# Kernel tuning notes

Hardware: AMD Instinct MI355X
Metric: run time of the kernel (lower is better)

The kernel has to match this reference:

```python
import jax, jax.numpy as jnp
import numpy as np

NC, NP, H, E, EL = 4096, 8192, 128, 500000, 500000


def setup_inputs() -> dict:
    key = jax.random.key(0)
    ks = jax.random.split(key, 32)
    W = lambda i, shape: jax.random.normal(ks[i], shape, dtype=jnp.float32) * 0.02
    inp = {
        "x_country": jax.random.normal(ks[0], (NC, NC), dtype=jnp.float32),
        "x_product": jax.random.normal(ks[1], (NP, NP), dtype=jnp.float32),
        # input projections (Linear(num_x, hidden)) and node-id embeddings
        "Wc_lin": W(2, (NC, H)), "bc_lin": jnp.zeros((H,), jnp.float32),
        "Wp_lin": W(3, (NP, H)), "bp_lin": jnp.zeros((H,), jnp.float32),
        "emb_c": W(4, (NC, H)),
        "emb_p": W(5, (NP, H)),
        # SAGEConv params per layer per edge type (lin_l has bias, lin_r does not)
        "W1ep_l": W(6, (H, H)), "b1ep": jnp.zeros((H,), jnp.float32), "W1ep_r": W(7, (H, H)),
        "W1pc_l": W(8, (H, H)), "b1pc": jnp.zeros((H,), jnp.float32), "W1pc_r": W(9, (H, H)),
        "W2ep_l": W(10, (H, H)), "b2ep": jnp.zeros((H,), jnp.float32), "W2ep_r": W(11, (H, H)),
        "W2pc_l": W(12, (H, H)), "b2pc": jnp.zeros((H,), jnp.float32), "W2pc_r": W(13, (H, H)),
        # graph structure
        "nid_c": jnp.arange(NC, dtype=jnp.int32),
        "nid_p": jnp.arange(NP, dtype=jnp.int32),
        "e_src": jax.random.randint(ks[14], (E,), 0, NC, dtype=jnp.int32),
        "e_dst": jax.random.randint(ks[15], (E,), 0, NP, dtype=jnp.int32),
        "l_src": jax.random.randint(ks[16], (EL,), 0, NC, dtype=jnp.int32),
        "l_dst": jax.random.randint(ks[17], (EL,), 0, NP, dtype=jnp.int32),
    }
    return inp


def _seg_mean(x, src, dst, n):
    # mean aggregation of source-node features onto destination nodes
    s = jax.ops.segment_sum(x[src], dst, num_segments=n)  # [n, H]
    c = jax.ops.segment_sum(jnp.ones_like(dst, dtype=x.dtype), dst, num_segments=n)
    return s / jnp.maximum(c, 1.0)[:, None]


def _sage(x_src, x_dst, src, dst, Wl, bl, Wr):
    # PyG SAGEConv(mean): lin_l(mean_agg(x_j)) + lin_r(x_i)
    return _seg_mean(x_src, src, dst, x_dst.shape[0]) @ Wl + bl + x_dst @ Wr


def reference(x_country, x_product, Wc_lin, bc_lin, Wp_lin, bp_lin, emb_c, emb_p,
              W1ep_l, b1ep, W1ep_r, W1pc_l, b1pc, W1pc_r,
              W2ep_l, b2ep, W2ep_r, W2pc_l, b2pc, W2pc_r,
              nid_c, nid_p, e_src, e_dst, l_src, l_dst):
    # input fusion: linear(features) + embedding(node_id)
    xc = x_country @ Wc_lin + bc_lin + emb_c[nid_c]  # [NC, H]
    xp = x_product @ Wp_lin + bp_lin + emb_p[nid_p]  # [NP, H]
    # hetero layer 1 (relu per node type); rev edges are the transpose of exports
    hp = jax.nn.relu(_sage(xc, xp, e_src, e_dst, W1ep_l, b1ep, W1ep_r))
    hc = jax.nn.relu(_sage(xp, xc, e_dst, e_src, W1pc_l, b1pc, W1pc_r))
    # hetero layer 2 (no relu)
    hp2 = _sage(hc, hp, e_src, e_dst, W2ep_l, b2ep, W2ep_r)
    hc2 = _sage(hp, hc, e_dst, e_src, W2pc_l, b2pc, W2pc_r)
    # edge-wise dot-product classifier over label edges
    return jnp.sum(hc2[l_src] * hp2[l_dst], axis=-1)  # [EL]
```

## Files before the change

### kernel.cpp

```cpp
#include <hip/hip_runtime.h>
#include <stdint.h>

#define NCn 4096
#define NPn 8192
#define Hn  128
#define En  500000
#define ELn 500000

typedef unsigned short u16;
using f32x4  = __attribute__((ext_vector_type(4))) float;
using bf16x8 = __attribute__((ext_vector_type(8))) short;

__device__ inline u16 f2bf(float f) {
  union { float f; uint32_t u; } v; v.f = f;
  uint32_t r = v.u + 0x7fffu + ((v.u >> 16) & 1u);
  return (u16)(r >> 16);
}

__global__ __launch_bounds__(256) void wtrans(const float* __restrict__ W,
                                              u16* __restrict__ WT, int K) {
  int t = blockIdx.x * 256 + threadIdx.x;
  int kc8 = K >> 3;
  if (t >= 128 * kc8) return;
  int kc = t % kc8, n = t / kc8;
  u16 pk[8];
#pragma unroll
  for (int j = 0; j < 8; ++j) pk[j] = f2bf(W[(size_t)(kc * 8 + j) * 128 + n]);
  uint4 v;
  v.x = (uint32_t)pk[0] | ((uint32_t)pk[1] << 16);
  v.y = (uint32_t)pk[2] | ((uint32_t)pk[3] << 16);
  v.z = (uint32_t)pk[4] | ((uint32_t)pk[5] << 16);
  v.w = (uint32_t)pk[6] | ((uint32_t)pk[7] << 16);
  *(uint4*)&WT[(size_t)n * K + kc * 8] = v;
}

__global__ __launch_bounds__(256) void count_deg(const int* __restrict__ esrc,
                                                 const int* __restrict__ edst,
                                                 int* __restrict__ cntC,
                                                 int* __restrict__ cntP) {
  int i = blockIdx.x * 256 + threadIdx.x;
  if (i >= En) return;
  atomicAdd(&cntP[edst[i]], 1);
  atomicAdd(&cntC[esrc[i]], 1);
}

__global__ __launch_bounds__(256) void scan_excl(const int* __restrict__ cnt,
                                                 int* __restrict__ off,
                                                 int* __restrict__ cur, int n) {
  __shared__ int sh[257];
  int t = threadIdx.x;
  int chunk = n >> 8;
  int base = t * chunk;
  int s = 0;
  for (int i = 0; i < chunk; ++i) s += cnt[base + i];
  sh[t] = s;
  __syncthreads();
  if (t == 0) {
    int run = 0;
    for (int i = 0; i < 256; ++i) { int v = sh[i]; sh[i] = run; run += v; }
    sh[256] = run;
  }
  __syncthreads();
  int p = sh[t];
  for (int i = 0; i < chunk; ++i) {
    off[base + i] = p; cur[base + i] = p; p += cnt[base + i];
  }
  if (t == 255) off[n] = sh[256];
}

__global__ __launch_bounds__(256) void fill_adj(const int* __restrict__ esrc,
                                                const int* __restrict__ edst,
                                                int* __restrict__ curC,
                                                int* __restrict__ curP,
                                                int* __restrict__ adjC,
                                                int* __restrict__ adjP) {
  int i = blockIdx.x * 256 + threadIdx.x;
  if (i >= En) return;
  int s = esrc[i], d = edst[i];
  int p = atomicAdd(&curP[d], 1);
  adjP[p] = s;
  int q = atomicAdd(&curC[s], 1);
  adjC[q] = d;
}

__global__ __launch_bounds__(256) void gemm_big(const float* __restrict__ A,
                                                const u16* __restrict__ BT,
                                                const float* __restrict__ bias,
                                                const float* __restrict__ addend,
                                                float* __restrict__ out, int K) {
  __shared__ __align__(16) u16 aL[32 * 64];
  __shared__ __align__(16) u16 bL[128 * 64];
  const int t = threadIdx.x;
  const int wid = t >> 6, lane = t & 63;
  const int ln15 = lane & 15, lhi = lane >> 4;
  const int m0 = blockIdx.x * 32;

  f32x4 acc[2][2] = {};

  const int ar0 = t >> 4;
  const int ac4 = t & 15;

  const int nIter = K >> 6;
  float4 av[2];
#pragma unroll
  for (int i = 0; i < 2; ++i)
    av[i] = *(const float4*)&A[(size_t)(m0 + ar0 + i * 16) * K + ac4 * 4];

  for (int it = 0; it < nIter; ++it) {
    const int k0 = it << 6;
    __syncthreads();
#pragma unroll
    for (int i = 0; i < 2; ++i) {
      int row = ar0 + i * 16;
      int off = row * 128 + ((ac4 * 8) ^ ((row & 7) << 4));
      uint2 p;
      p.x = (uint32_t)f2bf(av[i].x) | ((uint32_t)f2bf(av[i].y) << 16);
      p.y = (uint32_t)f2bf(av[i].z) | ((uint32_t)f2bf(av[i].w) << 16);
      *(uint2*)((char*)aL + off) = p;
    }
#pragma unroll
    for (int i = 0; i < 4; ++i) {
      int idx = t + i * 256;
      int n = idx >> 3, sl = idx & 7;
      const char* src = (const char*)BT + ((size_t)n * K + k0) * 2 + sl * 16;
      uint4 v = *(const uint4*)src;
      *(uint4*)((char*)bL + n * 128 + ((sl * 16) ^ ((n & 7) << 4))) = v;
    }
    if (it + 1 < nIter) {
#pragma unroll
      for (int i = 0; i < 2; ++i)
        av[i] = *(const float4*)&A[(size_t)(m0 + ar0 + i * 16) * K + (k0 + 64) + ac4 * 4];
    }
    __syncthreads();
#pragma unroll
    for (int ks = 0; ks < 2; ++ks) {
      const int kb = ks * 64 + lhi * 16;
      bf16x8 afr[2], bfr[2];
#pragma unroll
      for (int mi = 0; mi < 2; ++mi) {
        int r = mi * 16 + ln15;
        afr[mi] = *(const bf16x8*)((const char*)aL + r * 128 + (kb ^ ((r & 7) << 4)));
      }
#pragma unroll
      for (int ni = 0; ni < 2; ++ni) {
        int n = wid * 32 + ni * 16 + ln15;
        bfr[ni] = *(const bf16x8*)((const char*)bL + n * 128 + (kb ^ ((n & 7) << 4)));
      }
#pragma unroll
      for (int mi = 0; mi < 2; ++mi)
#pragma unroll
        for (int ni = 0; ni < 2; ++ni)
          acc[mi][ni] = __builtin_amdgcn_mfma_f32_16x16x32_bf16(afr[mi], bfr[ni],
                                                                acc[mi][ni], 0, 0, 0);
    }
  }
#pragma unroll
  for (int mi = 0; mi < 2; ++mi) {
#pragma unroll
    for (int ni = 0; ni < 2; ++ni) {
      int col = wid * 32 + ni * 16 + ln15;
      float bcol = bias[col];
#pragma unroll
      for (int r = 0; r < 4; ++r) {
        int row = m0 + mi * 16 + lhi * 4 + r;
        out[(size_t)row * 128 + col] = acc[mi][ni][r] + bcol + addend[(size_t)row * 128 + col];
      }
    }
  }
}

template <int RELU>
__global__ __launch_bounds__(256) void gemm_layer(const float* __restrict__ A1,
                                                  const float* __restrict__ A2,
                                                  const float* __restrict__ Wl,
                                                  const float* __restrict__ Wr,
                                                  const float* __restrict__ bias,
                                                  float* __restrict__ out) {
  __shared__ float aT[32][33];
  __shared__ float wT[32][128];
  const int t = threadIdx.x;
  const int tx = t & 15, ty = t >> 4;
  const int m0 = blockIdx.x * 32;
  float acc[2][8] = {};

  for (int kc = 0; kc < 8; ++kc) {
    const float* Asrc = (kc < 4) ? A1 : A2;
    const float* Wsrc = (kc < 4) ? Wl : Wr;
    const int kb = (kc & 3) * 32;
    __syncthreads();
    {
      int row = t >> 3, c4 = t & 7;
      float4 v = *(const float4*)&Asrc[(size_t)(m0 + row) * 128 + kb + c4 * 4];
      aT[row][c4 * 4 + 0] = v.x; aT[row][c4 * 4 + 1] = v.y;
      aT[row][c4 * 4 + 2] = v.z; aT[row][c4 * 4 + 3] = v.w;
    }
#pragma unroll
    for (int i = 0; i < 4; ++i) {
      int idx = t + i * 256;
      int row = idx >> 5, c4 = idx & 31;
      float4 v = *(const float4*)&Wsrc[(size_t)(kb + row) * 128 + c4 * 4];
      *(float4*)&wT[row][c4 * 4] = v;
    }
    __syncthreads();
#pragma unroll
    for (int k = 0; k < 32; ++k) {
      float a0 = aT[ty * 2 + 0][k], a1 = aT[ty * 2 + 1][k];
      float4 w0 = *(const float4*)&wT[k][tx * 8];
      float4 w1 = *(const float4*)&wT[k][tx * 8 + 4];
      float w[8] = {w0.x, w0.y, w0.z, w0.w, w1.x, w1.y, w1.z, w1.w};
#pragma unroll
      for (int j = 0; j < 8; ++j) {
        acc[0][j] += a0 * w[j];
        acc[1][j] += a1 * w[j];
      }
    }
  }
#pragma unroll
  for (int i = 0; i < 2; ++i) {
    int row = m0 + ty * 2 + i;
    float o[8];
#pragma unroll
    for (int j = 0; j < 8; ++j) {
      float v = acc[i][j] + bias[tx * 8 + j];
      o[j] = RELU ? fmaxf(v, 0.f) : v;
    }
    float4 v0 = {o[0], o[1], o[2], o[3]}, v1 = {o[4], o[5], o[6], o[7]};
    *(float4*)&out[(size_t)row * 128 + tx * 8] = v0;
    *(float4*)&out[(size_t)row * 128 + tx * 8 + 4] = v1;
  }
}

__global__ __launch_bounds__(256) void agg_mean(const int* __restrict__ adj,
                                                const int* __restrict__ off,
                                                const float* __restrict__ X,
                                                float* __restrict__ out, int ndst) {
  int w = blockIdx.x * 4 + (threadIdx.x >> 6);
  if (w >= ndst) return;
  int lane = threadIdx.x & 63;
  int s0 = off[w], s1 = off[w + 1];
  int deg = s1 - s0;
  float a0 = 0.f, a1 = 0.f;
  for (int base = 0; base < deg; base += 64) {
    int my = base + lane;
    int sv = (my < deg) ? adj[s0 + my] : 0;
    int cnt = min(64, deg - base);
    int jj = 0;
    for (; jj + 4 <= cnt; jj += 4) {
      int n0 = __shfl(sv, jj), n1 = __shfl(sv, jj + 1);
      int n2 = __shfl(sv, jj + 2), n3 = __shfl(sv, jj + 3);
      float2 f0 = *(const float2*)&X[(size_t)n0 * 128 + lane * 2];
      float2 f1 = *(const float2*)&X[(size_t)n1 * 128 + lane * 2];
      float2 f2 = *(const float2*)&X[(size_t)n2 * 128 + lane * 2];
      float2 f3 = *(const float2*)&X[(size_t)n3 * 128 + lane * 2];
      a0 += (f0.x + f1.x) + (f2.x + f3.x);
      a1 += (f0.y + f1.y) + (f2.y + f3.y);
    }
    for (; jj < cnt; ++jj) {
      int n = __shfl(sv, jj);
      float2 f = *(const float2*)&X[(size_t)n * 128 + lane * 2];
      a0 += f.x; a1 += f.y;
    }
  }
  float inv = 1.f / (float)max(deg, 1);
  float2 r; r.x = a0 * inv; r.y = a1 * inv;
  *(float2*)&out[(size_t)w * 128 + lane * 2] = r;
}

__global__ __launch_bounds__(256) void edge_dot(const int* __restrict__ ls,
                                                const int* __restrict__ ld,
                                                const float* __restrict__ hc2,
                                                const float* __restrict__ hp2,
                                                float* __restrict__ o, int n) {
  int w = blockIdx.x * 4 + (threadIdx.x >> 6);
  if (w >= n) return;
  int lane = threadIdx.x & 63;
  int s = ls[w], d = ld[w];
  float2 a = *(const float2*)&hc2[(size_t)s * 128 + lane * 2];
  float2 b = *(const float2*)&hp2[(size_t)d * 128 + lane * 2];
  float p = a.x * b.x + a.y * b.y;
#pragma unroll
  for (int m = 32; m; m >>= 1) p += __shfl_xor(p, m);
  if (lane == 0) o[w] = p;
}

extern "C" void kernel_launch(void* const* d_in, const int* in_sizes, int n_in,
                              void* d_out, int out_size, void* d_ws, size_t ws_size,
                              hipStream_t stream) {
  const float* x_c    = (const float*)d_in[0];
  const float* x_p    = (const float*)d_in[1];
  const float* Wc     = (const float*)d_in[2];
  const float* bc     = (const float*)d_in[3];
  const float* Wp     = (const float*)d_in[4];
  const float* bp     = (const float*)d_in[5];
  const float* emb_c  = (const float*)d_in[6];
  const float* emb_p  = (const float*)d_in[7];
  const float* W1ep_l = (const float*)d_in[8];
  const float* b1ep   = (const float*)d_in[9];
  const float* W1ep_r = (const float*)d_in[10];
  const float* W1pc_l = (const float*)d_in[11];
  const float* b1pc   = (const float*)d_in[12];
  const float* W1pc_r = (const float*)d_in[13];
  const float* W2ep_l = (const float*)d_in[14];
  const float* b2ep   = (const float*)d_in[15];
  const float* W2ep_r = (const float*)d_in[16];
  const float* W2pc_l = (const float*)d_in[17];
  const float* b2pc   = (const float*)d_in[18];
  const float* W2pc_r = (const float*)d_in[19];
  const int* e_src    = (const int*)d_in[22];
  const int* e_dst    = (const int*)d_in[23];
  const int* l_src    = (const int*)d_in[24];
  const int* l_dst    = (const int*)d_in[25];

  size_t off = 0;
  auto alloc = [&](size_t bytes) -> void* {
    void* p = (char*)d_ws + off;
    off += (bytes + 255) & ~(size_t)255;
    return p;
  };
  float* xc   = (float*)alloc((size_t)NCn * Hn * 4);
  float* xp   = (float*)alloc((size_t)NPn * Hn * 4);
  float* aggP = (float*)alloc((size_t)NPn * Hn * 4);
  float* aggC = (float*)alloc((size_t)NCn * Hn * 4);
  float* hp   = (float*)alloc((size_t)NPn * Hn * 4);
  float* hc   = (float*)alloc((size_t)NCn * Hn * 4);
  float* hp2  = (float*)alloc((size_t)NPn * Hn * 4);
  float* hc2  = (float*)alloc((size_t)NCn * Hn * 4);
  u16*   WcT  = (u16*)alloc((size_t)Hn * NCn * 2);
  u16*   WpT  = (u16*)alloc((size_t)Hn * NPn * 2);
  int*   adjP = (int*)alloc((size_t)En * 4);
  int*   adjC = (int*)alloc((size_t)En * 4);
  int*   offP = (int*)alloc((size_t)(NPn + 1) * 4);
  int*   offC = (int*)alloc((size_t)(NCn + 1) * 4);
  int*   curP = (int*)alloc((size_t)NPn * 4);
  int*   curC = (int*)alloc((size_t)NCn * 4);
  int*   cnts = (int*)alloc((size_t)(NPn + NCn) * 4);
  int*   cntP = cnts;
  int*   cntC = cnts + NPn;

  hipMemsetAsync(cnts, 0, (size_t)(NPn + NCn) * 4, stream);

  wtrans<<<(128 * (NCn >> 3) + 255) / 256, 256, 0, stream>>>(Wc, WcT, NCn);
  wtrans<<<(128 * (NPn >> 3) + 255) / 256, 256, 0, stream>>>(Wp, WpT, NPn);

  count_deg<<<(En + 255) / 256, 256, 0, stream>>>(e_src, e_dst, cntC, cntP);
  scan_excl<<<1, 256, 0, stream>>>(cntP, offP, curP, NPn);
  scan_excl<<<1, 256, 0, stream>>>(cntC, offC, curC, NCn);
  fill_adj<<<(En + 255) / 256, 256, 0, stream>>>(e_src, e_dst, curC, curP, adjC, adjP);

  gemm_big<<<NCn / 32, 256, 0, stream>>>(x_c, WcT, bc, emb_c, xc, NCn);
  gemm_big<<<NPn / 32, 256, 0, stream>>>(x_p, WpT, bp, emb_p, xp, NPn);

  agg_mean<<<NPn / 4, 256, 0, stream>>>(adjP, offP, xc, aggP, NPn);
  agg_mean<<<NCn / 4, 256, 0, stream>>>(adjC, offC, xp, aggC, NCn);
  gemm_layer<1><<<NPn / 32, 256, 0, stream>>>(aggP, xp, W1ep_l, W1ep_r, b1ep, hp);
  gemm_layer<1><<<NCn / 32, 256, 0, stream>>>(aggC, xc, W1pc_l, W1pc_r, b1pc, hc);

  agg_mean<<<NPn / 4, 256, 0, stream>>>(adjP, offP, hc, aggP, NPn);
  agg_mean<<<NCn / 4, 256, 0, stream>>>(adjC, offC, hp, aggC, NCn);
  gemm_layer<0><<<NPn / 32, 256, 0, stream>>>(aggP, hp, W2ep_l, W2ep_r, b2ep, hp2);
  gemm_layer<0><<<NCn / 32, 256, 0, stream>>>(aggC, hc, W2pc_l, W2pc_r, b2pc, hc2);

  edge_dot<<<(ELn + 3) / 4, 256, 0, stream>>>(l_src, l_dst, hc2, hp2, (float*)d_out, ELn);
}
```

Measured before the change: 929.4 us.

## Split-K big input GEMMs, register-prefetch tiles, widen gather loads to float4

The large input projections are split along K into 4 and 8 chunks over a 2D grid, which gives far more blocks than the 128/256 row blocks used before. A separate combine kernel sums the partials and adds bias and embedding. Both GEMM kernels now prefetch the next B/W tile into registers while the current tile is consumed. The aggregation and edge-dot kernels use 128-bit loads, with half-warps handling separate neighbors or edges. In exchange, the split-K path writes and rereads extra partial buffers (about 40 MB) and adds two launches.

```diff
diff --git a/kernel.cpp b/kernel.cpp
--- a/kernel.cpp
+++ b/kernel.cpp
@@ -83,31 +83,37 @@
   adjC[q] = d;
 }
 
-__global__ __launch_bounds__(256) void gemm_big(const float* __restrict__ A,
-                                                const u16* __restrict__ BT,
-                                                const float* __restrict__ bias,
-                                                const float* __restrict__ addend,
-                                                float* __restrict__ out, int K) {
+__global__ __launch_bounds__(256) void gemm_big_sk(const float* __restrict__ A,
+                                                   const u16* __restrict__ BT,
+                                                   float* __restrict__ part,
+                                                   int K, int Kc) {
   __shared__ __align__(16) u16 aL[32 * 64];
   __shared__ __align__(16) u16 bL[128 * 64];
   const int t = threadIdx.x;
   const int wid = t >> 6, lane = t & 63;
   const int ln15 = lane & 15, lhi = lane >> 4;
   const int m0 = blockIdx.x * 32;
+  const int kb0 = blockIdx.y * Kc;
+  const size_t M128 = (size_t)gridDim.x * 32 * 128;
 
   f32x4 acc[2][2] = {};
 
   const int ar0 = t >> 4;
   const int ac4 = t & 15;
-
-  const int nIter = K >> 6;
+  const int nIter = Kc >> 6;
+
   float4 av[2];
+  uint4  bv[4];
 #pragma unroll
   for (int i = 0; i < 2; ++i)
-    av[i] = *(const float4*)&A[(size_t)(m0 + ar0 + i * 16) * K + ac4 * 4];
+    av[i] = *(const float4*)&A[(size_t)(m0 + ar0 + i * 16) * K + kb0 + ac4 * 4];
+#pragma unroll
+  for (int i = 0; i < 4; ++i) {
+    int idx = t + i * 256, n = idx >> 3, sl = idx & 7;
+    bv[i] = *(const uint4*)((const char*)BT + ((size_t)n * K + kb0) * 2 + sl * 16);
+  }
 
   for (int it = 0; it < nIter; ++it) {
-    const int k0 = it << 6;
     __syncthreads();
 #pragma unroll
     for (int i = 0; i < 2; ++i) {
@@ -120,16 +126,19 @@
     }
 #pragma unroll
     for (int i = 0; i < 4; ++i) {
-      int idx = t + i * 256;
-      int n = idx >> 3, sl = idx & 7;
-      const char* src = (const char*)BT + ((size_t)n * K + k0) * 2 + sl * 16;
-      uint4 v = *(const uint4*)src;
-      *(uint4*)((char*)bL + n * 128 + ((sl * 16) ^ ((n & 7) << 4))) = v;
+      int idx = t + i * 256, n = idx >> 3, sl = idx & 7;
+      *(uint4*)((char*)bL + n * 128 + ((sl * 16) ^ ((n & 7) << 4))) = bv[i];
     }
     if (it + 1 < nIter) {
+      const int k0 = kb0 + (it + 1) * 64;
 #pragma unroll
       for (int i = 0; i < 2; ++i)
-        av[i] = *(const float4*)&A[(size_t)(m0 + ar0 + i * 16) * K + (k0 + 64) + ac4 * 4];
+        av[i] = *(const float4*)&A[(size_t)(m0 + ar0 + i * 16) * K + k0 + ac4 * 4];
+#pragma unroll
+      for (int i = 0; i < 4; ++i) {
+        int idx = t + i * 256, n = idx >> 3, sl = idx & 7;
+        bv[i] = *(const uint4*)((const char*)BT + ((size_t)n * K + k0) * 2 + sl * 16);
+      }
     }
     __syncthreads();
 #pragma unroll
@@ -154,19 +163,37 @@
                                                                 acc[mi][ni], 0, 0, 0);
     }
   }
+  float* P = part + (size_t)blockIdx.y * M128;
 #pragma unroll
   for (int mi = 0; mi < 2; ++mi) {
 #pragma unroll
     for (int ni = 0; ni < 2; ++ni) {
       int col = wid * 32 + ni * 16 + ln15;
-      float bcol = bias[col];
 #pragma unroll
       for (int r = 0; r < 4; ++r) {
         int row = m0 + mi * 16 + lhi * 4 + r;
-        out[(size_t)row * 128 + col] = acc[mi][ni][r] + bcol + addend[(size_t)row * 128 + col];
-      }
-    }
-  }
+        P[(size_t)row * 128 + col] = acc[mi][ni][r];
+      }
+    }
+  }
+}
+
+__global__ __launch_bounds__(256) void gemm_combine(const float* __restrict__ part,
+                                                    const float* __restrict__ bias,
+                                                    const float* __restrict__ addend,
+                                                    float* __restrict__ out,
+                                                    int M, int SK) {
+  int i = blockIdx.x * 256 + threadIdx.x;
+  int n4 = M * 32;
+  if (i >= n4) return;
+  size_t stride = (size_t)M * 128;
+  f32x4 s = {};
+  for (int c = 0; c < SK; ++c) s += *(const f32x4*)&part[c * stride + (size_t)i * 4];
+  int col = (i * 4) & 127;
+  f32x4 b = *(const f32x4*)&bias[col];
+  f32x4 ad = *(const f32x4*)&addend[(size_t)i * 4];
+  f32x4 r = s + b + ad;
+  *(f32x4*)&out[(size_t)i * 4] = r;
 }
 
 template <int RELU>
@@ -181,25 +208,32 @@
   const int t = threadIdx.x;
   const int tx = t & 15, ty = t >> 4;
   const int m0 = blockIdx.x * 32;
+  const int arow = t >> 3, ac = t & 7;
+  const int wrow8 = t >> 5, wc = t & 31;
   float acc[2][8] = {};
 
+  float4 a_v;
+  float4 w_v[4];
+  a_v = *(const float4*)&A1[(size_t)(m0 + arow) * 128 + ac * 4];
+#pragma unroll
+  for (int i = 0; i < 4; ++i)
+    w_v[i] = *(const float4*)&Wl[(size_t)(i * 8 + wrow8) * 128 + wc * 4];
+
   for (int kc = 0; kc < 8; ++kc) {
-    const float* Asrc = (kc < 4) ? A1 : A2;
-    const float* Wsrc = (kc < 4) ? Wl : Wr;
-    const int kb = (kc & 3) * 32;
     __syncthreads();
-    {
-      int row = t >> 3, c4 = t & 7;
-      float4 v = *(const float4*)&Asrc[(size_t)(m0 + row) * 128 + kb + c4 * 4];
-      aT[row][c4 * 4 + 0] = v.x; aT[row][c4 * 4 + 1] = v.y;
-      aT[row][c4 * 4 + 2] = v.z; aT[row][c4 * 4 + 3] = v.w;
-    }
-#pragma unroll
-    for (int i = 0; i < 4; ++i) {
-      int idx = t + i * 256;
-      int row = idx >> 5, c4 = idx & 31;
-      float4 v = *(const float4*)&Wsrc[(size_t)(kb + row) * 128 + c4 * 4];
-      *(float4*)&wT[row][c4 * 4] = v;
+    aT[arow][ac * 4 + 0] = a_v.x; aT[arow][ac * 4 + 1] = a_v.y;
+    aT[arow][ac * 4 + 2] = a_v.z; aT[arow][ac * 4 + 3] = a_v.w;
+#pragma unroll
+    for (int i = 0; i < 4; ++i) *(float4*)&wT[i * 8 + wrow8][wc * 4] = w_v[i];
+    if (kc + 1 < 8) {
+      int nk = kc + 1;
+      const float* Asrc = (nk < 4) ? A1 : A2;
+      const float* Wsrc = (nk < 4) ? Wl : Wr;
+      int kb = (nk & 3) * 32;
+      a_v = *(const float4*)&Asrc[(size_t)(m0 + arow) * 128 + kb + ac * 4];
+#pragma unroll
+      for (int i = 0; i < 4; ++i)
+        w_v[i] = *(const float4*)&Wsrc[(size_t)(kb + i * 8 + wrow8) * 128 + wc * 4];
     }
     __syncthreads();
 #pragma unroll
@@ -237,33 +271,38 @@
   int w = blockIdx.x * 4 + (threadIdx.x >> 6);
   if (w >= ndst) return;
   int lane = threadIdx.x & 63;
-  int s0 = off[w], s1 = off[w + 1];
-  int deg = s1 - s0;
-  float a0 = 0.f, a1 = 0.f;
+  int h = lane >> 5, c = lane & 31;
+  int s0 = off[w], deg = off[w + 1] - s0;
+  f32x4 acc0 = {}, acc1 = {};
   for (int base = 0; base < deg; base += 64) {
     int my = base + lane;
     int sv = (my < deg) ? adj[s0 + my] : 0;
     int cnt = min(64, deg - base);
     int jj = 0;
     for (; jj + 4 <= cnt; jj += 4) {
-      int n0 = __shfl(sv, jj), n1 = __shfl(sv, jj + 1);
-      int n2 = __shfl(sv, jj + 2), n3 = __shfl(sv, jj + 3);
-      float2 f0 = *(const float2*)&X[(size_t)n0 * 128 + lane * 2];
-      float2 f1 = *(const float2*)&X[(size_t)n1 * 128 + lane * 2];
-      float2 f2 = *(const float2*)&X[(size_t)n2 * 128 + lane * 2];
-      float2 f3 = *(const float2*)&X[(size_t)n3 * 128 + lane * 2];
-      a0 += (f0.x + f1.x) + (f2.x + f3.x);
-      a1 += (f0.y + f1.y) + (f2.y + f3.y);
-    }
-    for (; jj < cnt; ++jj) {
-      int n = __shfl(sv, jj);
-      float2 f = *(const float2*)&X[(size_t)n * 128 + lane * 2];
-      a0 += f.x; a1 += f.y;
-    }
-  }
-  float inv = 1.f / (float)max(deg, 1);
-  float2 r; r.x = a0 * inv; r.y = a1 * inv;
-  *(float2*)&out[(size_t)w * 128 + lane * 2] = r;
+      int n0 = __shfl(sv, jj + h);
+      int n1 = __shfl(sv, jj + 2 + h);
+      f32x4 f0 = *(const f32x4*)&X[(size_t)n0 * 128 + c * 4];
+      f32x4 f1 = *(const f32x4*)&X[(size_t)n1 * 128 + c * 4];
+      acc0 += f0; acc1 += f1;
+    }
+    for (; jj < cnt; jj += 2) {
+      int idx = jj + h;
+      int n = __shfl(sv, min(idx, cnt - 1));
+      if (idx < cnt) {
+        f32x4 f = *(const f32x4*)&X[(size_t)n * 128 + c * 4];
+        acc0 += f;
+      }
+    }
+  }
+  f32x4 acc = acc0 + acc1;
+#pragma unroll
+  for (int j = 0; j < 4; ++j) acc[j] += __shfl_xor(acc[j], 32);
+  if (h == 0) {
+    float inv = 1.f / (float)max(deg, 1);
+    acc *= inv;
+    *(f32x4*)&out[(size_t)w * 128 + c * 4] = acc;
+  }
 }
 
 __global__ __launch_bounds__(256) void edge_dot(const int* __restrict__ ls,
@@ -272,15 +311,17 @@
                                                 const float* __restrict__ hp2,
                                                 float* __restrict__ o, int n) {
   int w = blockIdx.x * 4 + (threadIdx.x >> 6);
-  if (w >= n) return;
   int lane = threadIdx.x & 63;
-  int s = ls[w], d = ld[w];
-  float2 a = *(const float2*)&hc2[(size_t)s * 128 + lane * 2];
-  float2 b = *(const float2*)&hp2[(size_t)d * 128 + lane * 2];
-  float p = a.x * b.x + a.y * b.y;
-#pragma unroll
-  for (int m = 32; m; m >>= 1) p += __shfl_xor(p, m);
-  if (lane == 0) o[w] = p;
+  int h = lane >> 5, c = lane & 31;
+  int e = w * 2 + h;
+  if (e >= n) return;
+  int s = ls[e], d = ld[e];
+  f32x4 a = *(const f32x4*)&hc2[(size_t)s * 128 + c * 4];
+  f32x4 b = *(const f32x4*)&hp2[(size_t)d * 128 + c * 4];
+  float p = a[0] * b[0] + a[1] * b[1] + a[2] * b[2] + a[3] * b[3];
+#pragma unroll
+  for (int m = 16; m; m >>= 1) p += __shfl_xor(p, m);
+  if (c == 0) o[e] = p;
 }
 
 extern "C" void kernel_launch(void* const* d_in, const int* in_sizes, int n_in,
@@ -317,25 +358,27 @@
     off += (bytes + 255) & ~(size_t)255;
     return p;
   };
-  float* xc   = (float*)alloc((size_t)NCn * Hn * 4);
-  float* xp   = (float*)alloc((size_t)NPn * Hn * 4);
-  float* aggP = (float*)alloc((size_t)NPn * Hn * 4);
-  float* aggC = (float*)alloc((size_t)NCn * Hn * 4);
-  float* hp   = (float*)alloc((size_t)NPn * Hn * 4);
-  float* hc   = (float*)alloc((size_t)NCn * Hn * 4);
-  float* hp2  = (float*)alloc((size_t)NPn * Hn * 4);
-  float* hc2  = (float*)alloc((size_t)NCn * Hn * 4);
-  u16*   WcT  = (u16*)alloc((size_t)Hn * NCn * 2);
-  u16*   WpT  = (u16*)alloc((size_t)Hn * NPn * 2);
-  int*   adjP = (int*)alloc((size_t)En * 4);
-  int*   adjC = (int*)alloc((size_t)En * 4);
-  int*   offP = (int*)alloc((size_t)(NPn + 1) * 4);
-  int*   offC = (int*)alloc((size_t)(NCn + 1) * 4);
-  int*   curP = (int*)alloc((size_t)NPn * 4);
-  int*   curC = (int*)alloc((size_t)NCn * 4);
-  int*   cnts = (int*)alloc((size_t)(NPn + NCn) * 4);
-  int*   cntP = cnts;
-  int*   cntC = cnts + NPn;
+  float* xc    = (float*)alloc((size_t)NCn * Hn * 4);
+  float* xp    = (float*)alloc((size_t)NPn * Hn * 4);
+  float* aggP  = (float*)alloc((size_t)NPn * Hn * 4);
+  float* aggC  = (float*)alloc((size_t)NCn * Hn * 4);
+  float* hp    = (float*)alloc((size_t)NPn * Hn * 4);
+  float* hc    = (float*)alloc((size_t)NCn * Hn * 4);
+  float* hp2   = (float*)alloc((size_t)NPn * Hn * 4);
+  float* hc2   = (float*)alloc((size_t)NCn * Hn * 4);
+  u16*   WcT   = (u16*)alloc((size_t)Hn * NCn * 2);
+  u16*   WpT   = (u16*)alloc((size_t)Hn * NPn * 2);
+  float* partP = (float*)alloc((size_t)8 * NPn * Hn * 4);
+  float* partC = (float*)alloc((size_t)4 * NCn * Hn * 4);
+  int*   adjP  = (int*)alloc((size_t)En * 4);
+  int*   adjC  = (int*)alloc((size_t)En * 4);
+  int*   offP  = (int*)alloc((size_t)(NPn + 1) * 4);
+  int*   offC  = (int*)alloc((size_t)(NCn + 1) * 4);
+  int*   curP  = (int*)alloc((size_t)NPn * 4);
+  int*   curC  = (int*)alloc((size_t)NCn * 4);
+  int*   cnts  = (int*)alloc((size_t)(NPn + NCn) * 4);
+  int*   cntP  = cnts;
+  int*   cntC  = cnts + NPn;
 
   hipMemsetAsync(cnts, 0, (size_t)(NPn + NCn) * 4, stream);
 
@@ -347,8 +390,10 @@
   scan_excl<<<1, 256, 0, stream>>>(cntC, offC, curC, NCn);
   fill_adj<<<(En + 255) / 256, 256, 0, stream>>>(e_src, e_dst, curC, curP, adjC, adjP);
 
-  gemm_big<<<NCn / 32, 256, 0, stream>>>(x_c, WcT, bc, emb_c, xc, NCn);
-  gemm_big<<<NPn / 32, 256, 0, stream>>>(x_p, WpT, bp, emb_p, xp, NPn);
+  gemm_big_sk<<<dim3(NCn / 32, 4), 256, 0, stream>>>(x_c, WcT, partC, NCn, NCn / 4);
+  gemm_big_sk<<<dim3(NPn / 32, 8), 256, 0, stream>>>(x_p, WpT, partP, NPn, NPn / 8);
+  gemm_combine<<<(NCn * 32 + 255) / 256, 256, 0, stream>>>(partC, bc, emb_c, xc, NCn, 4);
+  gemm_combine<<<(NPn * 32 + 255) / 256, 256, 0, stream>>>(partP, bp, emb_p, xp, NPn, 8);
 
   agg_mean<<<NPn / 4, 256, 0, stream>>>(adjP, offP, xc, aggP, NPn);
   agg_mean<<<NCn / 4, 256, 0, stream>>>(adjC, offC, xp, aggC, NCn);
@@ -360,5 +405,5 @@
   gemm_layer<0><<<NPn / 32, 256, 0, stream>>>(aggP, hp, W2ep_l, W2ep_r, b2ep, hp2);
   gemm_layer<0><<<NCn / 32, 256, 0, stream>>>(aggC, hc, W2pc_l, W2pc_r, b2pc, hc2);
 
-  edge_dot<<<(ELn + 3) / 4, 256, 0, stream>>>(l_src, l_dst, hc2, hp2, (float*)d_out, ELn);
-}
+  edge_dot<<<(ELn + 7) / 8, 256, 0, stream>>>(l_src, l_dst, hc2, hp2, (float*)d_out, ELn);
+}
```

New measurement: 1.053 ms. 13.3% more time.
